# Kernel tuning notes

Hardware: AMD Instinct MI355X
Metric: run time of the kernel (lower is better)

## Reference

```python
import jax, jax.numpy as jnp
import numpy as np

NUM_USER = 1000
NUM_NODES = 3000
NUM_REL = 5
HID = 500
OUT = 75
NUM_BASIS = 2
NUM_EDGES = 200000


def setup_inputs() -> dict:
    key = jax.random.key(0)
    ks = jax.random.split(key, 8)
    x = jnp.arange(NUM_NODES, dtype=jnp.int64 if jax.config.jax_enable_x64 else jnp.int32)
    edge_index = jax.random.randint(ks[0], (2, NUM_EDGES), 0, NUM_NODES)
    edge_type = jax.random.randint(ks[1], (NUM_EDGES,), 0, NUM_REL)
    edge_norm = jax.random.uniform(ks[2], (NUM_EDGES,), dtype=jnp.float32)
    # RGC ordinal basis weights: W_r = cumsum of per-relation bases (GCMC ordinal weight sharing)
    ord_basis = 0.01 * jax.random.normal(ks[3], (NUM_REL, NUM_NODES, HID), dtype=jnp.float32)
    # DenseLayer weight (no bias), shared for user/item branches
    W_dense = 0.05 * jax.random.normal(ks[4], (HID, OUT), dtype=jnp.float32)
    # BiDecoder basis decomposition
    basis_matrix = 0.1 * jax.random.normal(ks[5], (NUM_BASIS, OUT * OUT), dtype=jnp.float32)
    coefs = 0.1 * jax.random.normal(ks[6], (NUM_REL, NUM_BASIS), dtype=jnp.float32)
    return {"x": x, "edge_index": edge_index, "edge_type": edge_type,
            "edge_norm": edge_norm, "ord_basis": ord_basis, "W_dense": W_dense,
            "basis_matrix": basis_matrix, "coefs": coefs}


def reference(x, edge_index, edge_type, edge_norm, ord_basis, W_dense, basis_matrix, coefs):
    R, N, H = ord_basis.shape
    # --- RGCLayer: ordinal cumulative weight sharing ---
    weight = jnp.cumsum(ord_basis, axis=0).reshape(R * N, H)  # (R*N, H)
    src, dst = edge_index[0], edge_index[1]
    idx = edge_type * N + x[src]                      # row lookup = one-hot feature matmul
    msgs = weight[idx] * edge_norm[:, None]           # (E, H) gather, memory-bound
    agg = jax.ops.segment_sum(msgs, dst, num_segments=N)  # scatter-add to target nodes
    feat = jax.nn.relu(agg)                           # (N, H)
    # --- separate users / items, DenseLayer ---
    u = jax.nn.relu(feat[:NUM_USER] @ W_dense)        # (U, OUT)
    i = jax.nn.relu(feat[NUM_USER:] @ W_dense)        # (I, OUT)
    # --- BiDecoder: basis-combination bilinear scores per relation ---
    D = W_dense.shape[1]
    Q = jnp.einsum('rb,bk->rk', coefs, basis_matrix).reshape(R, D, D)
    out = jnp.einsum('ud,rde,ie->uir', u, Q, i)       # (U, I, R)
    return out.reshape(u.shape[0] * i.shape[0], R)
```

## Files before the change

### kernel.cpp

```cpp
#include <hip/hip_runtime.h>
#include <hip/hip_bf16.h>

#define NUSER 1000
#define NNODES 3000
#define NREL 5
#define HID 500
#define DOUT 75
#define NBASIS 2
#define NEDGES 200000
#define NITEM (NNODES - NUSER)
#define NH (NNODES * HID)

__global__ void k_cumsum(const float4* __restrict__ basis, float4* __restrict__ weight,
                         int* __restrict__ deg) {
    int i = blockIdx.x * blockDim.x + threadIdx.x;
    if (i < NNODES) deg[i] = 0;
    if (i >= NH / 4) return;
    float4 s = make_float4(0.f, 0.f, 0.f, 0.f);
#pragma unroll
    for (int r = 0; r < NREL; ++r) {
        float4 b = basis[r * (NH / 4) + i];
        s.x += b.x; s.y += b.y; s.z += b.z; s.w += b.w;
        weight[r * (NH / 4) + i] = s;
    }
}

__global__ void k_degree(const int* __restrict__ dst, int* __restrict__ deg) {
    int e = blockIdx.x * blockDim.x + threadIdx.x;
    if (e < NEDGES) atomicAdd(&deg[dst[e]], 1);
}

__global__ __launch_bounds__(1024) void k_scan(const int* __restrict__ deg,
                                               int* __restrict__ offs,
                                               int* __restrict__ cursor) {
    __shared__ int wsum[16];
    int t = threadIdx.x;
    int base = t * 3;
    int a = (base     < NNODES) ? deg[base]     : 0;
    int b = (base + 1 < NNODES) ? deg[base + 1] : 0;
    int c = (base + 2 < NNODES) ? deg[base + 2] : 0;
    int s = a + b + c;
    int lane = t & 63, wid = t >> 6;
    int v = s;
#pragma unroll
    for (int d = 1; d < 64; d <<= 1) {
        int x = __shfl_up(v, d);
        if (lane >= d) v += x;
    }
    if (lane == 63) wsum[wid] = v;
    __syncthreads();
    if (t < 16) {
        int w = wsum[t];
#pragma unroll
        for (int d = 1; d < 16; d <<= 1) {
            int x = __shfl_up(w, d);
            if (t >= d) w += x;
        }
        wsum[t] = w;
    }
    __syncthreads();
    int woff = wid ? wsum[wid - 1] : 0;
    int incl = v + woff;
    int excl = incl - s;
    if (base < NNODES)     { offs[base]     = excl;         cursor[base]     = excl; }
    if (base + 1 < NNODES) { offs[base + 1] = excl + a;     cursor[base + 1] = excl + a; }
    if (base + 2 < NNODES) { offs[base + 2] = excl + a + b; cursor[base + 2] = excl + a + b; }
    if (t == 1023) offs[NNODES] = incl;
}

__global__ void k_fill(const int* __restrict__ src, const int* __restrict__ dst,
                       const int* __restrict__ etype, const float* __restrict__ enorm,
                       const int* __restrict__ x,
                       int* __restrict__ cursor, int* __restrict__ csr_row,
                       float* __restrict__ csr_norm) {
    int e = blockIdx.x * blockDim.x + threadIdx.x;
    if (e >= NEDGES) return;
    int d = dst[e];
    int pos = atomicAdd(&cursor[d], 1);
    csr_row[pos] = etype[e] * NNODES + x[src[e]];
    csr_norm[pos] = enorm[e];
}

__global__ __launch_bounds__(256) void k_agg(const float4* __restrict__ w4,
                                             const int* __restrict__ offs,
                                             const int* __restrict__ csr_row,
                                             const float* __restrict__ csr_norm,
                                             float4* __restrict__ feat4) {
    __shared__ float4 part[125];
    int n = blockIdx.x;
    int t = threadIdx.x;
    int beg = offs[n], end = offs[n + 1];
    int half = t >> 7;
    int lane = t & 127;
    float4 acc = make_float4(0.f, 0.f, 0.f, 0.f);
    if (lane < 125) {
        for (int p = beg + half; p < end; p += 2) {
            int row = csr_row[p];
            float w = csr_norm[p];
            float4 v = w4[(size_t)row * 125 + lane];
            acc.x += v.x * w; acc.y += v.y * w; acc.z += v.z * w; acc.w += v.w * w;
        }
    }
    if (half == 1 && lane < 125) part[lane] = acc;
    __syncthreads();
    if (half == 0 && lane < 125) {
        float4 o = part[lane];
        acc.x = fmaxf(acc.x + o.x, 0.f);
        acc.y = fmaxf(acc.y + o.y, 0.f);
        acc.z = fmaxf(acc.z + o.z, 0.f);
        acc.w = fmaxf(acc.w + o.w, 0.f);
        feat4[(size_t)n * 125 + lane] = acc;
    }
}

#define DN 8
__global__ __launch_bounds__(256) void k_dense(const float* __restrict__ feat,
                                               const float* __restrict__ W,
                                               float* __restrict__ uv) {
    __shared__ float lds[DN][HID];
    int nb = blockIdx.x * DN;
    int t = threadIdx.x;
    const float4* f4 = (const float4*)(feat + (size_t)nb * HID);
    float4* l4 = (float4*)&lds[0][0];
    for (int j = t; j < DN * HID / 4; j += 256) l4[j] = f4[j];
    __syncthreads();
    if (t < 225) {
        int g = t / 75, o = t % 75;
        float a0 = 0.f, a1 = 0.f, a2 = 0.f;
        for (int d = 0; d < HID; ++d) {
            float w = W[d * DOUT + o];
            a0 += lds[g][d] * w;
            a1 += lds[g + 3][d] * w;
            a2 += lds[(g + 6) & 7][d] * w;
        }
        uv[(nb + g) * DOUT + o]     = fmaxf(a0, 0.f);
        uv[(nb + g + 3) * DOUT + o] = fmaxf(a1, 0.f);
        if (g < 2) uv[(nb + g + 6) * DOUT + o] = fmaxf(a2, 0.f);
    }
}

__global__ void k_T(const float* __restrict__ uv, const float* __restrict__ bm,
                    float* __restrict__ T) {
    int i = blockIdx.x * blockDim.x + threadIdx.x;
    if (i >= NBASIS * NUSER * DOUT) return;
    int b = i / (NUSER * DOUT);
    int rem = i % (NUSER * DOUT);
    int u = rem / DOUT;
    int e = rem % DOUT;
    float acc = 0.f;
    for (int d = 0; d < DOUT; ++d)
        acc += uv[u * DOUT + d] * bm[b * DOUT * DOUT + d * DOUT + e];
    T[i] = acc;
}

#define UT 32
#define IT 128
#define EC 25
__global__ __launch_bounds__(256) void k_dec(const float* __restrict__ T,
                                             const float* __restrict__ uv,
                                             const float* __restrict__ coefs,
                                             float* __restrict__ out) {
    __shared__ float As[NBASIS][UT][EC];
    __shared__ float Is[IT][EC];
    int t = threadIdx.x;
    int ti = t & 31;
    int tu = t >> 5;
    int ub = blockIdx.y * UT;
    int ib = blockIdx.x * IT;

    float acc[NBASIS][4][4] = {};

    for (int e0 = 0; e0 < DOUT; e0 += EC) {
        for (int j = t; j < NBASIS * UT * EC; j += 256) {
            int b = j / (UT * EC);
            int rem = j % (UT * EC);
            int uu = rem / EC, c = rem % EC;
            int u = ub + uu;
            As[b][uu][c] = (u < NUSER) ? T[(b * NUSER + u) * DOUT + e0 + c] : 0.f;
        }
        for (int j = t; j < IT * EC; j += 256) {
            int ii = j / EC, c = j % EC;
            int i = ib + ii;
            Is[ii][c] = (i < NITEM) ? uv[(size_t)(NUSER + i) * DOUT + e0 + c] : 0.f;
        }
        __syncthreads();
        for (int c = 0; c < EC; ++c) {
            float av[NBASIS][4];
#pragma unroll
            for (int b = 0; b < NBASIS; ++b)
#pragma unroll
                for (int uu = 0; uu < 4; ++uu)
                    av[b][uu] = As[b][tu * 4 + uu][c];
            float iv[4];
#pragma unroll
            for (int k = 0; k < 4; ++k) iv[k] = Is[ti + 32 * k][c];
#pragma unroll
            for (int b = 0; b < NBASIS; ++b)
#pragma unroll
                for (int uu = 0; uu < 4; ++uu)
#pragma unroll
                    for (int k = 0; k < 4; ++k)
                        acc[b][uu][k] += av[b][uu] * iv[k];
        }
        __syncthreads();
    }

    float cf[NREL][NBASIS];
#pragma unroll
    for (int r = 0; r < NREL; ++r)
#pragma unroll
        for (int b = 0; b < NBASIS; ++b) cf[r][b] = coefs[r * NBASIS + b];

#pragma unroll
    for (int uu = 0; uu < 4; ++uu) {
        int u = ub + tu * 4 + uu;
        if (u >= NUSER) continue;
#pragma unroll
        for (int k = 0; k < 4; ++k) {
            int i = ib + ti + 32 * k;
            if (i >= NITEM) continue;
            size_t base = ((size_t)u * NITEM + i) * NREL;
            float s0 = acc[0][uu][k], s1 = acc[1][uu][k];
#pragma unroll
            for (int r = 0; r < NREL; ++r)
                out[base + r] = cf[r][0] * s0 + cf[r][1] * s1;
        }
    }
}

extern "C" void kernel_launch(void* const* d_in, const int* in_sizes, int n_in,
                              void* d_out, int out_size, void* d_ws, size_t ws_size,
                              hipStream_t stream) {
    const int*   x     = (const int*)d_in[0];
    const int*   ei    = (const int*)d_in[1];
    const int*   etype = (const int*)d_in[2];
    const float* enorm = (const float*)d_in[3];
    const float* basis = (const float*)d_in[4];
    const float* Wd    = (const float*)d_in[5];
    const float* bm    = (const float*)d_in[6];
    const float* coefs = (const float*)d_in[7];
    float* out = (float*)d_out;

    float* weight   = (float*)d_ws;
    float* feat     = weight + 7500000;
    float* uv       = feat + 1500000;
    float* T        = uv + 225000;
    float* csr_norm = T + 150000;
    int*   csr_row  = (int*)(csr_norm + 200000);
    int*   deg      = csr_row + 200000;
    int*   offs     = deg + 3000;
    int*   cursor   = offs + 3001;

    const int* src = ei;
    const int* dst = ei + NEDGES;

    k_cumsum<<<(NH / 4 + 255) / 256, 256, 0, stream>>>((const float4*)basis,
                                                       (float4*)weight, deg);
    k_degree<<<(NEDGES + 255) / 256, 256, 0, stream>>>(dst, deg);
    k_scan<<<1, 1024, 0, stream>>>(deg, offs, cursor);
    k_fill<<<(NEDGES + 255) / 256, 256, 0, stream>>>(src, dst, etype, enorm, x, cursor,
                                                     csr_row, csr_norm);
    k_agg<<<NNODES, 256, 0, stream>>>((const float4*)weight, offs, csr_row, csr_norm,
                                      (float4*)feat);
    k_dense<<<NNODES / DN, 256, 0, stream>>>(feat, Wd, uv);
    k_T<<<(NBASIS * NUSER * DOUT + 255) / 256, 256, 0, stream>>>(uv, bm, T);
    k_dec<<<dim3((NITEM + IT - 1) / IT, (NUSER + UT - 1) / UT), 256, 0, stream>>>(T, uv, coefs, out);
}
```

Measured before the change: 273.4 us.

## Split aggregation per node across 8 column slices with 16 edge groups

```diff
diff --git a/kernel.cpp b/kernel.cpp
--- a/kernel.cpp
+++ b/kernel.cpp
@@ -10,6 +10,7 @@
 #define NEDGES 200000
 #define NITEM (NNODES - NUSER)
 #define NH (NNODES * HID)
+#define ROWF4 125
 
 __global__ void k_cumsum(const float4* __restrict__ basis, float4* __restrict__ weight,
                          int* __restrict__ deg) {
@@ -86,30 +87,42 @@
                                              const int* __restrict__ csr_row,
                                              const float* __restrict__ csr_norm,
                                              float4* __restrict__ feat4) {
-    __shared__ float4 part[125];
-    int n = blockIdx.x;
-    int t = threadIdx.x;
+    __shared__ float4 part[16][16];
+    int bid = blockIdx.x;
+    int s = bid & 7;
+    int n = bid >> 3;
+    int t = threadIdx.x;
+    int g = t >> 4;
+    int lane = t & 15;
+    int wdt = (s < 7) ? 16 : 13;
+    int boff = s * 16;
     int beg = offs[n], end = offs[n + 1];
-    int half = t >> 7;
-    int lane = t & 127;
     float4 acc = make_float4(0.f, 0.f, 0.f, 0.f);
-    if (lane < 125) {
-        for (int p = beg + half; p < end; p += 2) {
+    if (lane < wdt) {
+        for (int p = beg + g; p < end; p += 16) {
             int row = csr_row[p];
-            float w = csr_norm[p];
-            float4 v = w4[(size_t)row * 125 + lane];
-            acc.x += v.x * w; acc.y += v.y * w; acc.z += v.z * w; acc.w += v.w * w;
-        }
-    }
-    if (half == 1 && lane < 125) part[lane] = acc;
-    __syncthreads();
-    if (half == 0 && lane < 125) {
-        float4 o = part[lane];
-        acc.x = fmaxf(acc.x + o.x, 0.f);
-        acc.y = fmaxf(acc.y + o.y, 0.f);
-        acc.z = fmaxf(acc.z + o.z, 0.f);
-        acc.w = fmaxf(acc.w + o.w, 0.f);
-        feat4[(size_t)n * 125 + lane] = acc;
+            float wn = csr_norm[p];
+            float4 v = w4[(size_t)row * ROWF4 + boff + lane];
+            acc.x += v.x * wn; acc.y += v.y * wn; acc.z += v.z * wn; acc.w += v.w * wn;
+        }
+    }
+    part[g][lane] = acc;
+    __syncthreads();
+#pragma unroll
+    for (int st = 8; st >= 1; st >>= 1) {
+        if (g < st) {
+            float4 o = part[g + st][lane];
+            float4 m = part[g][lane];
+            m.x += o.x; m.y += o.y; m.z += o.z; m.w += o.w;
+            part[g][lane] = m;
+        }
+        __syncthreads();
+    }
+    if (g == 0 && lane < wdt) {
+        float4 m = part[0][lane];
+        m.x = fmaxf(m.x, 0.f); m.y = fmaxf(m.y, 0.f);
+        m.z = fmaxf(m.z, 0.f); m.w = fmaxf(m.w, 0.f);
+        feat4[(size_t)n * ROWF4 + boff + lane] = m;
     }
 }
 
@@ -260,8 +273,8 @@
     k_scan<<<1, 1024, 0, stream>>>(deg, offs, cursor);
     k_fill<<<(NEDGES + 255) / 256, 256, 0, stream>>>(src, dst, etype, enorm, x, cursor,
                                                      csr_row, csr_norm);
-    k_agg<<<NNODES, 256, 0, stream>>>((const float4*)weight, offs, csr_row, csr_norm,
-                                      (float4*)feat);
+    k_agg<<<NNODES * 8, 256, 0, stream>>>((const float4*)weight, offs, csr_row, csr_norm,
+                                          (float4*)feat);
     k_dense<<<NNODES / DN, 256, 0, stream>>>(feat, Wd, uv);
     k_T<<<(NBASIS * NUSER * DOUT + 255) / 256, 256, 0, stream>>>(uv, bm, T);
     k_dec<<<dim3((NITEM + IT - 1) / IT, (NUSER + UT - 1) / UT), 256, 0, stream>>>(T, uv, coefs, out);
```

Measured after the change: 262.7 us. 3.9% less time.
